# Optimization experiments

Hardware: AMD Instinct MI355X
Metric: run time of the kernel (lower is better)

Reference implementation:

```python
import jax, jax.numpy as jnp
import numpy as np

B, T, C, NH, L, V = 2, 1024, 768, 12, 4, 50304
HS = C // NH  # 64


def _norm(x):
    # torch: (x - x.mean(-1)) / x.std(-1) with unbiased std (ddof=1)
    mu = jnp.mean(x, axis=-1, keepdims=True)
    sd = jnp.std(x, axis=-1, ddof=1, keepdims=True)
    return (x - mu) / sd


def setup_inputs() -> dict:
    key = jax.random.key(0)
    ks = jax.random.split(key, 8)
    idx = jax.random.randint(ks[0], (B, T), 0, V)
    wte = jax.random.normal(ks[1], (V, C), jnp.float32) * 0.02
    wpe = jax.random.normal(ks[2], (1024, C), jnp.float32) * 0.02
    c_attn_w = jax.random.normal(ks[3], (L, 3 * C, C), jnp.float32) * 0.02
    c_proj_w = jax.random.normal(ks[4], (L, C, C), jnp.float32) * 0.02
    w_decay = jax.random.uniform(ks[5], (L, C), jnp.float32)          # decay in [0,1)
    eta = jax.random.uniform(ks[6], (L, C), jnp.float32) * 0.01       # small, like 1/block_size init
    lm_head_w = jax.random.normal(ks[7], (V, C), jnp.float32) * 0.02
    return dict(idx=idx, wte=wte, wpe=wpe, c_attn_w=c_attn_w, c_proj_w=c_proj_w,
                w_decay=w_decay, eta=eta, lm_head_w=lm_head_w)


def _rwkv7_block(x, Wqkv, Wproj, wd, et):
    Bx, Tx, Cx = x.shape
    qkv = (x @ Wqkv.T).reshape(Bx, Tx, 3, NH, HS)
    qkv = _norm(qkv)
    # [T, B, nh, hs] each
    q = jnp.transpose(qkv[:, :, 0], (1, 0, 2, 3))
    k = jnp.transpose(qkv[:, :, 1], (1, 0, 2, 3))
    v = jnp.transpose(qkv[:, :, 2], (1, 0, 2, 3))
    q = jax.lax.erf(q)
    k = jax.lax.erf(k)
    wv = wd.reshape(NH, HS)   # decay per (head, channel i)
    ev = et.reshape(NH, HS)
    a = -k
    b = k * ev
    k_ = k * ev
    v_ = v

    def step(state, inp):
        q_t, a_t, b_t, k_t, v_t = inp
        # state: [B, nh, hs(i), hs(k)]
        sab = jnp.einsum('bhik,bhk,bhj->bhij', state, a_t, b_t)
        state = state * wv[None, :, :, None] + sab + jnp.einsum('bhj,bhi->bhij', k_t, v_t)
        out = jnp.einsum('bhj,bhij->bhi', q_t, state)
        return state, out

    state0 = jnp.zeros((Bx, NH, HS, HS), x.dtype)
    _, vt = jax.lax.scan(step, state0, (q, a, b, k_, v_))  # vt: [T, B, nh, hs]
    y = jnp.transpose(vt, (1, 0, 2, 3)).reshape(Bx, Tx, Cx) @ Wproj.T
    return x + y


def reference(idx, wte, wpe, c_attn_w, c_proj_w, w_decay, eta, lm_head_w):
    t = idx.shape[1]
    x = wte[idx] + wpe[:t][None]
    for l in range(L):
        x = _rwkv7_block(x, c_attn_w[l], c_proj_w[l], w_decay[l], eta[l])
    x = _norm(x)
    # targets=None path: logits for last position only
    logits = x[:, -1:, :] @ lm_head_w.T  # [B, 1, V]
    return logits
```

## Files before the change

kernel.cpp:

```cpp
#include <hip/hip_runtime.h>
#include <hip/hip_bf16.h>
#include <cmath>

using bf16   = __bf16;
using bf16x8 = __attribute__((ext_vector_type(8))) __bf16;
using bf16x4 = __attribute__((ext_vector_type(4))) __bf16;
using f32x4  = __attribute__((ext_vector_type(4))) float;
using u32x4  = __attribute__((ext_vector_type(4))) unsigned int;

__global__ __launch_bounds__(256) void prologue_kernel(const int* __restrict__ idx,
                                                       const float* __restrict__ wte,
                                                       const float* __restrict__ wpe,
                                                       const float* __restrict__ c_attn_w,
                                                       const float* __restrict__ c_proj_w,
                                                       float* __restrict__ xf,
                                                       bf16* __restrict__ xb,
                                                       bf16* __restrict__ WqB,
                                                       bf16* __restrict__ WpB) {
  const int bid = blockIdx.x, tid = threadIdx.x;
  if (bid < 2048) {
    int t = bid & 1023;
    int tok = idx[bid];
    const float* wr = wte + (long)tok * 768;
    const float* pr = wpe + (long)t * 768;
    for (int c = tid; c < 768; c += 256) {
      float v = wr[c] + pr[c];
      xf[(long)bid * 768 + c] = v;
      xb[(long)bid * 768 + c] = (bf16)v;
    }
  }
  const int n4a = 4 * 2304 * 768 / 4;
  for (int i = bid * 256 + tid; i < n4a; i += 4096 * 256) {
    f32x4 v = ((const f32x4*)c_attn_w)[i];
    bf16x4 o;
    o[0] = (bf16)v[0]; o[1] = (bf16)v[1]; o[2] = (bf16)v[2]; o[3] = (bf16)v[3];
    ((bf16x4*)WqB)[i] = o;
  }
  const int n4p = 4 * 768 * 768 / 4;
  for (int i = bid * 256 + tid; i < n4p; i += 4096 * 256) {
    f32x4 v = ((const f32x4*)c_proj_w)[i];
    bf16x4 o;
    o[0] = (bf16)v[0]; o[1] = (bf16)v[1]; o[2] = (bf16)v[2]; o[3] = (bf16)v[3];
    ((bf16x4*)WpB)[i] = o;
  }
}

__global__ __launch_bounds__(256) void gemmqkv_kernel(const bf16* __restrict__ A,
                                                      const bf16* __restrict__ W,
                                                      const float* __restrict__ eta_l,
                                                      bf16* __restrict__ qG,
                                                      bf16* __restrict__ aG,
                                                      bf16* __restrict__ bG,
                                                      float* __restrict__ vG) {
  __shared__ char ldsA[128 * 128];
  __shared__ char ldsB[128 * 128];
  const int tid = threadIdx.x;
  const int l = tid & 63, wid = tid >> 6;
  const int lr = l & 15, g = l >> 4;
  const int m0 = blockIdx.y * 128, n0 = blockIdx.x * 128;
  const int wm = wid >> 1, wn = wid & 1;
  const int K = 768;

  f32x4 acc[4][4];
#pragma unroll
  for (int i = 0; i < 4; ++i)
#pragma unroll
    for (int j = 0; j < 4; ++j) acc[i][j] = {0.f, 0.f, 0.f, 0.f};

  for (int k0 = 0; k0 < K; k0 += 32) {
    __syncthreads();
#pragma unroll
    for (int it = 0; it < 2; ++it) {
      int slot = tid + it * 256;
      int row = slot >> 2, q = slot & 3;
      u32x4 da = *(const u32x4*)(A + (long)(m0 + row) * K + k0 + q * 8);
      *(u32x4*)(ldsA + row * 128 + ((q * 16) ^ ((row & 7) << 4))) = da;
      u32x4 db = *(const u32x4*)(W + (long)(n0 + row) * K + k0 + q * 8);
      *(u32x4*)(ldsB + row * 128 + ((q * 16) ^ ((row & 7) << 4))) = db;
    }
    __syncthreads();
    bf16x8 af[4], bfr[4];
#pragma unroll
    for (int it = 0; it < 4; ++it) {
      int row = wm * 64 + it * 16 + lr;
      af[it] = *(const bf16x8*)(ldsA + row * 128 + ((16 * g) ^ ((row & 7) << 4)));
    }
#pragma unroll
    for (int jt = 0; jt < 4; ++jt) {
      int row = wn * 64 + jt * 16 + lr;
      bfr[jt] = *(const bf16x8*)(ldsB + row * 128 + ((16 * g) ^ ((row & 7) << 4)));
    }
#pragma unroll
    for (int it = 0; it < 4; ++it)
#pragma unroll
      for (int jt = 0; jt < 4; ++jt)
        acc[it][jt] = __builtin_amdgcn_mfma_f32_16x16x32_bf16(af[it], bfr[jt], acc[it][jt], 0, 0, 0);
  }

  const int gi = blockIdx.x * 2 + wn;
  const int s = gi / 12, h = gi - s * 12;
  float evc[4];
#pragma unroll
  for (int jt = 0; jt < 4; ++jt) evc[jt] = eta_l[h * 64 + jt * 16 + lr];

#pragma unroll
  for (int it = 0; it < 4; ++it) {
#pragma unroll
    for (int r = 0; r < 4; ++r) {
      int row = m0 + wm * 64 + it * 16 + g * 4 + r;
      int b = row >> 10, t = row & 1023;
      float x0 = acc[it][0][r], x1 = acc[it][1][r];
      float x2 = acc[it][2][r], x3 = acc[it][3][r];
      float sum = (x0 + x1) + (x2 + x3);
#pragma unroll
      for (int o = 8; o; o >>= 1) sum += __shfl_xor(sum, o);
      float mu = sum * (1.f / 64.f);
      float d0 = x0 - mu, d1 = x1 - mu, d2 = x2 - mu, d3 = x3 - mu;
      float v2 = (d0 * d0 + d1 * d1) + (d2 * d2 + d3 * d3);
#pragma unroll
      for (int o = 8; o; o >>= 1) v2 += __shfl_xor(v2, o);
      float sd = sqrtf(v2 * (1.f / 63.f));
      float gn0 = d0 / sd, gn1 = d1 / sd, gn2 = d2 / sd, gn3 = d3 / sd;
      long base = ((long)(b * 12 + h) * 1024 + t) * 64 + lr;
      if (s == 0) {
        qG[base]      = (bf16)erff(gn0);
        qG[base + 16] = (bf16)erff(gn1);
        qG[base + 32] = (bf16)erff(gn2);
        qG[base + 48] = (bf16)erff(gn3);
      } else if (s == 1) {
        float k0 = erff(gn0), k1 = erff(gn1), k2 = erff(gn2), k3 = erff(gn3);
        aG[base]      = (bf16)(-k0);
        aG[base + 16] = (bf16)(-k1);
        aG[base + 32] = (bf16)(-k2);
        aG[base + 48] = (bf16)(-k3);
        bG[base]      = (bf16)(k0 * evc[0]);
        bG[base + 16] = (bf16)(k1 * evc[1]);
        bG[base + 32] = (bf16)(k2 * evc[2]);
        bG[base + 48] = (bf16)(k3 * evc[3]);
      } else {
        vG[base]      = gn0;
        vG[base + 16] = gn1;
        vG[base + 32] = gn2;
        vG[base + 48] = gn3;
      }
    }
  }
}

__global__ __launch_bounds__(256) void gemmproj_kernel(const bf16* __restrict__ A,
                                                       const bf16* __restrict__ W,
                                                       float* __restrict__ xf,
                                                       bf16* __restrict__ xb) {
  __shared__ char ldsA[128 * 128];
  __shared__ char ldsB[128 * 128];
  const int tid = threadIdx.x;
  const int l = tid & 63, wid = tid >> 6;
  const int lr = l & 15, g = l >> 4;
  const int m0 = blockIdx.y * 128, n0 = blockIdx.x * 128;
  const int wm = wid >> 1, wn = wid & 1;
  const int K = 768;

  f32x4 acc[4][4];
#pragma unroll
  for (int i = 0; i < 4; ++i)
#pragma unroll
    for (int j = 0; j < 4; ++j) acc[i][j] = {0.f, 0.f, 0.f, 0.f};

  for (int k0 = 0; k0 < K; k0 += 32) {
    __syncthreads();
#pragma unroll
    for (int it = 0; it < 2; ++it) {
      int slot = tid + it * 256;
      int row = slot >> 2, q = slot & 3;
      u32x4 da = *(const u32x4*)(A + (long)(m0 + row) * K + k0 + q * 8);
      *(u32x4*)(ldsA + row * 128 + ((q * 16) ^ ((row & 7) << 4))) = da;
      u32x4 db = *(const u32x4*)(W + (long)(n0 + row) * K + k0 + q * 8);
      *(u32x4*)(ldsB + row * 128 + ((q * 16) ^ ((row & 7) << 4))) = db;
    }
    __syncthreads();
    bf16x8 af[4], bfr[4];
#pragma unroll
    for (int it = 0; it < 4; ++it) {
      int row = wm * 64 + it * 16 + lr;
      af[it] = *(const bf16x8*)(ldsA + row * 128 + ((16 * g) ^ ((row & 7) << 4)));
    }
#pragma unroll
    for (int jt = 0; jt < 4; ++jt) {
      int row = wn * 64 + jt * 16 + lr;
      bfr[jt] = *(const bf16x8*)(ldsB + row * 128 + ((16 * g) ^ ((row & 7) << 4)));
    }
#pragma unroll
    for (int it = 0; it < 4; ++it)
#pragma unroll
      for (int jt = 0; jt < 4; ++jt)
        acc[it][jt] = __builtin_amdgcn_mfma_f32_16x16x32_bf16(af[it], bfr[jt], acc[it][jt], 0, 0, 0);
  }

#pragma unroll
  for (int it = 0; it < 4; ++it) {
#pragma unroll
    for (int jt = 0; jt < 4; ++jt) {
      int col = n0 + wn * 64 + jt * 16 + lr;
#pragma unroll
      for (int r = 0; r < 4; ++r) {
        int row = m0 + wm * 64 + it * 16 + g * 4 + r;
        long o = (long)row * 768 + col;
        float v = acc[it][jt][r] + xf[o];
        xf[o] = v;
        xb[o] = (bf16)v;
      }
    }
  }
}

__global__ __launch_bounds__(256) void gram_kernel(const bf16* __restrict__ aG,
                                                   const bf16* __restrict__ bG,
                                                   const bf16* __restrict__ qG,
                                                   float* __restrict__ GaG,
                                                   bf16* __restrict__ GqG,
                                                   bf16* __restrict__ bTG) {
  const int bh = blockIdx.x >> 6, ch = blockIdx.x & 63;
  __shared__ float as[16][68], bs[16][68], qs[16][68];
  const long tb = ((long)bh * 1024 + ch * 16) * 64;
  for (int i = threadIdx.x; i < 1024; i += 256) {
    int t = i >> 6, d = i & 63;
    as[t][d] = (float)aG[tb + i];
    bs[t][d] = (float)bG[tb + i];
    qs[t][d] = (float)qG[tb + i];
  }
  __syncthreads();
  const int t = threadIdx.x & 15, u = threadIdx.x >> 4;
  float dba = 0.f, dbq = 0.f;
#pragma unroll 4
  for (int d = 0; d < 64; ++d) {
    float bv = bs[u][d];
    dba += bv * as[t][d];
    dbq += bv * qs[t][d];
  }
  long g2 = (long)bh * 64 + ch;
  GaG[g2 * 256 + u * 16 + t] = (u < t) ? dba : 0.f;
  GqG[g2 * 512 + t * 32 + u] = (u <= t) ? (bf16)dbq : (bf16)0.f;
  GqG[g2 * 512 + t * 32 + 16 + u] = (bf16)0.f;
  int jj = threadIdx.x >> 2, uq = threadIdx.x & 3;
  bf16x8 pkv;
#pragma unroll
  for (int uu = 0; uu < 8; ++uu) pkv[uu] = (uq < 2) ? (bf16)bs[uq * 8 + uu][jj] : (bf16)0.f;
  *(bf16x8*)(bTG + g2 * 2048 + jj * 32 + uq * 8) = pkv;
}

__global__ __launch_bounds__(256) void scan_kernel(const float* __restrict__ wdl,
                                                   const bf16* __restrict__ aG,
                                                   const bf16* __restrict__ qG,
                                                   const float* __restrict__ vG,
                                                   const float* __restrict__ GaG,
                                                   const bf16* __restrict__ GqG,
                                                   const bf16* __restrict__ bTG,
                                                   bf16* __restrict__ yG) {
  const int bh = blockIdx.x;
  const int b = bh / 12, h = bh - b * 12;
  const int tid = threadIdx.x;
  const int l = tid & 63, wid = tid >> 6;
  const int lr = l & 15, g = l >> 4;

  __shared__ char sA[2][2][16 * 128];
  __shared__ char sQ[2][2][16 * 128];
  __shared__ char sB[2][2][64 * 64];
  __shared__ char sG[2][2][16 * 64];
  __shared__ float sGa[2][2][16][16];
  __shared__ float sV[2][2][16][64];
  __shared__ char sS[64 * 128];
  __shared__ float sM[16][68];

  const float* wrow = wdl + h * 64;
  const int irow = wid * 16 + lr;
  const float w_rec = fmaxf(wrow[irow], 0.004f);
  const float winv = 1.0f / w_rec;

  float wc[4], w15c[4], l2wc[4];
#pragma unroll
  for (int r = 0; r < 4; ++r) {
    int row = wid * 16 + g * 4 + r;
    float w = fmaxf(wrow[row], 0.004f);
    wc[r] = w;
    l2wc[r] = log2f(w);
    w15c[r] = exp2f(15.0f * l2wc[r]);
  }

  f32x4 Sf[4];
#pragma unroll
  for (int j = 0; j < 4; ++j) Sf[j] = {0.f, 0.f, 0.f, 0.f};

  const long hTD = (long)bh * 65536;
  const long gB = (long)bh * 64;

  u32x4 rAQ[2], rB[2], rGG[2];
  f32x4 rV[2];

  auto LOAD2 = [&](int c0) {
#pragma unroll
    for (int k = 0; k < 2; ++k) {
      const int c = c0 + k;
      const long tb = hTD + (long)c * 1024;
      if (tid < 128) {
        rAQ[k] = *(const u32x4*)(aG + tb + (tid >> 3) * 64 + (tid & 7) * 8);
      } else {
        rAQ[k] = *(const u32x4*)(qG + tb + ((tid - 128) >> 3) * 64 + ((tid - 128) & 7) * 8);
      }
      rB[k] = *(const u32x4*)(bTG + (gB + c) * 2048 + (tid >> 2) * 32 + (tid & 3) * 8);
      if (tid < 64) {
        rGG[k] = *(const u32x4*)(GqG + (gB + c) * 512 + (tid >> 2) * 32 + (tid & 3) * 8);
      } else if (tid < 128) {
        rGG[k] = *(const u32x4*)(GaG + (gB + c) * 256 + ((tid - 64) >> 2) * 16 + ((tid - 64) & 3) * 4);
      }
      rV[k] = *(const f32x4*)(vG + tb + (tid >> 4) * 64 + (tid & 15) * 4);
    }
  };

  auto STORE2 = [&](int nb) {
#pragma unroll
    for (int k = 0; k < 2; ++k) {
      if (tid < 128) {
        int t = tid >> 3, q = tid & 7;
        *(u32x4*)(sA[nb][k] + t * 128 + ((q * 16) ^ ((t & 7) << 4))) = rAQ[k];
      } else {
        int t = (tid - 128) >> 3, q = (tid - 128) & 7;
        *(u32x4*)(sQ[nb][k] + t * 128 + ((q * 16) ^ ((t & 7) << 4))) = rAQ[k];
      }
      {
        int j = tid >> 2, q = tid & 3;
        *(u32x4*)(sB[nb][k] + j * 64 + ((q * 16) ^ ((j & 3) << 4))) = rB[k];
      }
      if (tid < 64) {
        int t = tid >> 2, q = tid & 3;
        *(u32x4*)(sG[nb][k] + t * 64 + ((q * 16) ^ ((t & 3) << 4))) = rGG[k];
      } else if (tid < 128) {
        int u = (tid - 64) >> 2, q = (tid - 64) & 3;
        *(u32x4*)(&sGa[nb][k][u][q * 4]) = rGG[k];
      }
      {
        int t = tid >> 4, i4 = tid & 15;
        *(f32x4*)(&sV[nb][k][t][i4 * 4]) = rV[k];
      }
    }
  };

  auto COMPUTE = [&](int cur, int cip, int ch) {
    const char* pA = sA[cur][cip];
    const char* pQ = sQ[cur][cip];
    const char* pB = sB[cur][cip];
    const char* pG = sG[cur][cip];
    const float* pGa = &sGa[cur][cip][0][0];
    const float* pV = &sV[cur][cip][0][0] + irow;
    const float* pM = &sM[0][0] + irow;

    asm volatile("s_waitcnt lgkmcnt(0)" ::: "memory");
    __builtin_amdgcn_sched_barrier(0);

    f32x4 mf = {0.f, 0.f, 0.f, 0.f}, mqf = {0.f, 0.f, 0.f, 0.f};
#pragma unroll
    for (int s = 0; s < 2; ++s) {
      bf16x8 af = *(const bf16x8*)(sS + irow * 128 + ((64 * s + 16 * g) ^ ((irow & 7) << 4)));
      bf16x8 ba = *(const bf16x8*)(pA + lr * 128 + ((64 * s + 16 * g) ^ ((lr & 7) << 4)));
      bf16x8 bq = *(const bf16x8*)(pQ + lr * 128 + ((64 * s + 16 * g) ^ ((lr & 7) << 4)));
      mf = __builtin_amdgcn_mfma_f32_16x16x32_bf16(af, ba, mf, 0, 0, 0);
      mqf = __builtin_amdgcn_mfma_f32_16x16x32_bf16(af, bq, mqf, 0, 0, 0);
    }
#pragma unroll
    for (int r = 0; r < 4; ++r) sM[lr][wid * 16 + g * 4 + r] = mf[r];
    asm volatile("s_waitcnt lgkmcnt(0)" ::: "memory");
    __builtin_amdgcn_sched_barrier(0);

    f32x4 acc4[4];
#pragma unroll
    for (int t = 0; t < 4; ++t) acc4[t] = {0.f, 0.f, 0.f, 0.f};
    bf16x8 zfrag;
#pragma unroll
    for (int i = 0; i < 8; ++i) zfrag[i] = (bf16)0.0f;
    float wp = 1.f, wpm1 = 0.f, wiv = 1.f;
#pragma unroll
    for (int u = 0; u < 16; ++u) {
      float muv = pM[u * 68];
      float vu = pV[u * 64];
      float cc = wp * muv + wpm1 * acc4[u >> 2][u & 3];
      float zt = wiv * (cc + vu);
      zfrag[u & 7] = (g == (u >> 3)) ? (bf16)zt : zfrag[u & 7];
      f32x4 ztv = {zt, zt, zt, zt};
#pragma unroll
      for (int qq = 0; qq < 4; ++qq) {
        f32x4 ga = *(const f32x4*)(pGa + u * 16 + qq * 4);
        acc4[qq] = __builtin_elementwise_fma(ga, ztv, acc4[qq]);
      }
      wpm1 = wp;
      wp *= w_rec;
      wiv *= winv;
    }

#pragma unroll
    for (int jt = 0; jt < 4; ++jt) {
      int jrow = jt * 16 + lr;
      bf16x8 bb = *(const bf16x8*)(pB + jrow * 64 + ((16 * g) ^ ((jrow & 3) << 4)));
      f32x4 cs;
#pragma unroll
      for (int r = 0; r < 4; ++r) cs[r] = Sf[jt][r] * wc[r];
      f32x4 ns = __builtin_amdgcn_mfma_f32_16x16x32_bf16(zfrag, bb, cs, 0, 0, 0);
#pragma unroll
      for (int r = 0; r < 4; ++r) Sf[jt][r] = ns[r] * w15c[r];
    }

#pragma unroll
    for (int jt = 0; jt < 4; ++jt) {
#pragma unroll
      for (int r = 0; r < 4; ++r) {
        int row = wid * 16 + g * 4 + r;
        int d = jt * 16 + lr;
        *(bf16*)(sS + row * 128 + ((d * 2) ^ ((row & 7) << 4))) = (bf16)Sf[jt][r];
      }
    }

    {
      bf16x8 gq = *(const bf16x8*)(pG + lr * 64 + ((16 * g) ^ ((lr & 3) << 4)));
      f32x4 cy;
#pragma unroll
      for (int r = 0; r < 4; ++r) cy[r] = mqf[r] * wc[r];
      f32x4 yp = __builtin_amdgcn_mfma_f32_16x16x32_bf16(zfrag, gq, cy, 0, 0, 0);
      bf16x4 yo;
#pragma unroll
      for (int r = 0; r < 4; ++r) yo[r] = (bf16)(yp[r] * exp2f((float)lr * l2wc[r]));
      long yoff = ((long)b * 1024 + ch * 16 + lr) * 768 + h * 64 + wid * 16 + g * 4;
      *(bf16x4*)(yG + yoff) = yo;
    }
  };

  LOAD2(0);
  STORE2(0);
#pragma unroll
  for (int jt = 0; jt < 4; ++jt) {
#pragma unroll
    for (int r = 0; r < 4; ++r) {
      int row = wid * 16 + g * 4 + r;
      int d = jt * 16 + lr;
      *(bf16*)(sS + row * 128 + ((d * 2) ^ ((row & 7) << 4))) = (bf16)0.0f;
    }
  }
  __syncthreads();

  for (int gp = 0; gp < 32; ++gp) {
    const int cur = gp & 1;
    if (gp < 31) LOAD2(2 * gp + 2);
    COMPUTE(cur, 0, 2 * gp);
    COMPUTE(cur, 1, 2 * gp + 1);
    if (gp < 31) STORE2(cur ^ 1);
    __syncthreads();
  }
}

__global__ __launch_bounds__(256) void lmhead_kernel(const float* __restrict__ W,
                                                     const float* __restrict__ xf,
                                                     float* __restrict__ out) {
  __shared__ float xn[2][768];
  __shared__ float red[4];
  const int tid = threadIdx.x;
  for (int b = 0; b < 2; ++b) {
    const float* xr = xf + ((long)b * 1024 + 1023) * 768;
    float s = 0.f;
    for (int c = tid; c < 768; c += 256) s += xr[c];
#pragma unroll
    for (int o = 32; o; o >>= 1) s += __shfl_xor(s, o);
    if ((tid & 63) == 0) red[tid >> 6] = s;
    __syncthreads();
    float mu = (red[0] + red[1] + red[2] + red[3]) * (1.f / 768.f);
    __syncthreads();
    float s2 = 0.f;
    for (int c = tid; c < 768; c += 256) {
      float d = xr[c] - mu;
      s2 += d * d;
    }
#pragma unroll
    for (int o = 32; o; o >>= 1) s2 += __shfl_xor(s2, o);
    if ((tid & 63) == 0) red[tid >> 6] = s2;
    __syncthreads();
    float sd = sqrtf((red[0] + red[1] + red[2] + red[3]) * (1.f / 767.f));
    for (int c = tid; c < 768; c += 256) xn[b][c] = (xr[c] - mu) / sd;
    __syncthreads();
  }

  int l = tid & 63, wid = tid >> 6;
  int v0 = blockIdx.x * 64 + wid * 16;
  f32x4 x0[3], x1[3];
#pragma unroll
  for (int i = 0; i < 3; ++i) {
    x0[i] = *(const f32x4*)(&xn[0][l * 4 + i * 256]);
    x1[i] = *(const f32x4*)(&xn[1][l * 4 + i * 256]);
  }
  for (int vi = 0; vi < 16; ++vi) {
    const float* wr = W + (long)(v0 + vi) * 768;
    float pa = 0.f, pb = 0.f;
#pragma unroll
    for (int i = 0; i < 3; ++i) {
      f32x4 wv = *(const f32x4*)(wr + l * 4 + i * 256);
#pragma unroll
      for (int r = 0; r < 4; ++r) {
        pa += wv[r] * x0[i][r];
        pb += wv[r] * x1[i][r];
      }
    }
#pragma unroll
    for (int o = 32; o; o >>= 1) {
      pa += __shfl_xor(pa, o);
      pb += __shfl_xor(pb, o);
    }
    if (l == 0) {
      out[v0 + vi] = pa;
      out[50304 + v0 + vi] = pb;
    }
  }
}

extern "C" void kernel_launch(void* const* d_in, const int* in_sizes, int n_in,
                              void* d_out, int out_size, void* d_ws, size_t ws_size,
                              hipStream_t stream) {
  (void)in_sizes; (void)n_in; (void)out_size; (void)ws_size;
  const int*   idx      = (const int*)d_in[0];
  const float* wte      = (const float*)d_in[1];
  const float* wpe      = (const float*)d_in[2];
  const float* c_attn_w = (const float*)d_in[3];
  const float* c_proj_w = (const float*)d_in[4];
  const float* w_decay  = (const float*)d_in[5];
  const float* eta      = (const float*)d_in[6];
  const float* lm_head  = (const float*)d_in[7];
  float* out = (float*)d_out;

  char* ws = (char*)d_ws;
  size_t off = 0;
  auto alloc = [&](size_t bytes) -> char* {
    char* p = ws + off;
    off = (off + bytes + 255) & ~(size_t)255;
    return p;
  };
  float* xf   = (float*)alloc(2L * 1024 * 768 * 4);
  bf16*  xb   = (bf16*)alloc(2L * 1024 * 768 * 2);
  bf16*  qGp  = (bf16*)alloc(24L * 1024 * 64 * 2);
  bf16*  aGp  = (bf16*)alloc(24L * 1024 * 64 * 2);
  bf16*  bGp  = (bf16*)alloc(24L * 1024 * 64 * 2);
  float* vGp  = (float*)alloc(24L * 1024 * 64 * 4);
  float* GaGp = (float*)alloc(24L * 64 * 256 * 4);
  bf16*  GqGp = (bf16*)alloc(24L * 64 * 512 * 2);
  bf16*  bTGp = (bf16*)alloc(24L * 64 * 2048 * 2);
  bf16*  yGp  = (bf16*)alloc(2L * 1024 * 768 * 2);
  bf16*  WqB  = (bf16*)alloc(4L * 2304 * 768 * 2);
  bf16*  WpB  = (bf16*)alloc(4L * 768 * 768 * 2);

  prologue_kernel<<<dim3(4096), dim3(256), 0, stream>>>(
      idx, wte, wpe, c_attn_w, c_proj_w, xf, xb, WqB, WpB);

  for (int l = 0; l < 4; ++l) {
    gemmqkv_kernel<<<dim3(18, 16), dim3(256), 0, stream>>>(
        xb, WqB + (long)l * 2304 * 768, eta + l * 768, qGp, aGp, bGp, vGp);
    gram_kernel<<<dim3(1536), dim3(256), 0, stream>>>(aGp, bGp, qGp, GaGp, GqGp, bTGp);
    scan_kernel<<<dim3(24), dim3(256), 0, stream>>>(
        w_decay + l * 768, aGp, qGp, vGp, GaGp, GqGp, bTGp, yGp);
    gemmproj_kernel<<<dim3(6, 16), dim3(256), 0, stream>>>(
        yGp, WpB + (long)l * 768 * 768, xf, xb);
  }

  lmhead_kernel<<<dim3(786), dim3(256), 0, stream>>>(lm_head, xf, out);
}
```

Baseline: 781.3 us.

## Load scan operands directly into MFMA fragments and drop per-chunk block barriers

```diff
diff --git a/kernel.cpp b/kernel.cpp
--- a/kernel.cpp
+++ b/kernel.cpp
@@ -51,7 +51,7 @@
                                                       bf16* __restrict__ qG,
                                                       bf16* __restrict__ aG,
                                                       bf16* __restrict__ bG,
-                                                      float* __restrict__ vG) {
+                                                      float* __restrict__ vT) {
   __shared__ char ldsA[128 * 128];
   __shared__ char ldsB[128 * 128];
   const int tid = threadIdx.x;
@@ -138,10 +138,12 @@
         bG[base + 32] = (bf16)(k2 * evc[2]);
         bG[base + 48] = (bf16)(k3 * evc[3]);
       } else {
-        vG[base]      = gn0;
-        vG[base + 16] = gn1;
-        vG[base + 32] = gn2;
-        vG[base + 48] = gn3;
+        long cb = ((long)(b * 12 + h) * 64 + (t >> 4)) * 1024;
+        int u = t & 15;
+        vT[cb + (lr)      * 16 + u] = gn0;
+        vT[cb + (16 + lr) * 16 + u] = gn1;
+        vT[cb + (32 + lr) * 16 + u] = gn2;
+        vT[cb + (48 + lr) * 16 + u] = gn3;
       }
     }
   }
@@ -251,7 +253,7 @@
 __global__ __launch_bounds__(256) void scan_kernel(const float* __restrict__ wdl,
                                                    const bf16* __restrict__ aG,
                                                    const bf16* __restrict__ qG,
-                                                   const float* __restrict__ vG,
+                                                   const float* __restrict__ vT,
                                                    const float* __restrict__ GaG,
                                                    const bf16* __restrict__ GqG,
                                                    const bf16* __restrict__ bTG,
@@ -262,14 +264,9 @@
   const int l = tid & 63, wid = tid >> 6;
   const int lr = l & 15, g = l >> 4;
 
-  __shared__ char sA[2][2][16 * 128];
-  __shared__ char sQ[2][2][16 * 128];
-  __shared__ char sB[2][2][64 * 64];
-  __shared__ char sG[2][2][16 * 64];
-  __shared__ float sGa[2][2][16][16];
-  __shared__ float sV[2][2][16][64];
-  __shared__ char sS[64 * 128];
+  __shared__ char  sS[64 * 128];
   __shared__ float sM[16][68];
+  __shared__ float sGaW[4][16][16];
 
   const float* wrow = wdl + h * 64;
   const int irow = wid * 16 + lr;
@@ -293,77 +290,46 @@
   const long hTD = (long)bh * 65536;
   const long gB = (long)bh * 64;
 
-  u32x4 rAQ[2], rB[2], rGG[2];
-  f32x4 rV[2];
-
-  auto LOAD2 = [&](int c0) {
-#pragma unroll
-    for (int k = 0; k < 2; ++k) {
-      const int c = c0 + k;
-      const long tb = hTD + (long)c * 1024;
-      if (tid < 128) {
-        rAQ[k] = *(const u32x4*)(aG + tb + (tid >> 3) * 64 + (tid & 7) * 8);
-      } else {
-        rAQ[k] = *(const u32x4*)(qG + tb + ((tid - 128) >> 3) * 64 + ((tid - 128) & 7) * 8);
-      }
-      rB[k] = *(const u32x4*)(bTG + (gB + c) * 2048 + (tid >> 2) * 32 + (tid & 3) * 8);
-      if (tid < 64) {
-        rGG[k] = *(const u32x4*)(GqG + (gB + c) * 512 + (tid >> 2) * 32 + (tid & 3) * 8);
-      } else if (tid < 128) {
-        rGG[k] = *(const u32x4*)(GaG + (gB + c) * 256 + ((tid - 64) >> 2) * 16 + ((tid - 64) & 3) * 4);
-      }
-      rV[k] = *(const f32x4*)(vG + tb + (tid >> 4) * 64 + (tid & 15) * 4);
-    }
+  struct Frag {
+    bf16x8 a0, a1, q0, q1, bt0, bt1, bt2, bt3, gq;
+    f32x4 v0, v1, v2, v3, ga;
   };
 
-  auto STORE2 = [&](int nb) {
-#pragma unroll
-    for (int k = 0; k < 2; ++k) {
-      if (tid < 128) {
-        int t = tid >> 3, q = tid & 7;
-        *(u32x4*)(sA[nb][k] + t * 128 + ((q * 16) ^ ((t & 7) << 4))) = rAQ[k];
-      } else {
-        int t = (tid - 128) >> 3, q = (tid - 128) & 7;
-        *(u32x4*)(sQ[nb][k] + t * 128 + ((q * 16) ^ ((t & 7) << 4))) = rAQ[k];
-      }
-      {
-        int j = tid >> 2, q = tid & 3;
-        *(u32x4*)(sB[nb][k] + j * 64 + ((q * 16) ^ ((j & 3) << 4))) = rB[k];
-      }
-      if (tid < 64) {
-        int t = tid >> 2, q = tid & 3;
-        *(u32x4*)(sG[nb][k] + t * 64 + ((q * 16) ^ ((t & 3) << 4))) = rGG[k];
-      } else if (tid < 128) {
-        int u = (tid - 64) >> 2, q = (tid - 64) & 3;
-        *(u32x4*)(&sGa[nb][k][u][q * 4]) = rGG[k];
-      }
-      {
-        int t = tid >> 4, i4 = tid & 15;
-        *(f32x4*)(&sV[nb][k][t][i4 * 4]) = rV[k];
-      }
-    }
+  auto LOADF = [&](int c, Frag& F) {
+    const long tb = hTD + (long)c * 1024;
+    const bf16* ap = aG + tb + lr * 64 + 8 * g;
+    F.a0 = *(const bf16x8*)(ap);
+    F.a1 = *(const bf16x8*)(ap + 32);
+    const bf16* qp = qG + tb + lr * 64 + 8 * g;
+    F.q0 = *(const bf16x8*)(qp);
+    F.q1 = *(const bf16x8*)(qp + 32);
+    const bf16* bp = bTG + (gB + c) * 2048 + lr * 32 + 8 * g;
+    F.bt0 = *(const bf16x8*)(bp);
+    F.bt1 = *(const bf16x8*)(bp + 512);
+    F.bt2 = *(const bf16x8*)(bp + 1024);
+    F.bt3 = *(const bf16x8*)(bp + 1536);
+    F.gq = *(const bf16x8*)(GqG + (gB + c) * 512 + lr * 32 + 8 * g);
+    const float* vp = vT + ((gB + c) * 64 + irow) * 16;
+    F.v0 = *(const f32x4*)(vp);
+    F.v1 = *(const f32x4*)(vp + 4);
+    F.v2 = *(const f32x4*)(vp + 8);
+    F.v3 = *(const f32x4*)(vp + 12);
+    F.ga = *(const f32x4*)(GaG + (gB + c) * 256 + l * 4);
   };
 
-  auto COMPUTE = [&](int cur, int cip, int ch) {
-    const char* pA = sA[cur][cip];
-    const char* pQ = sQ[cur][cip];
-    const char* pB = sB[cur][cip];
-    const char* pG = sG[cur][cip];
-    const float* pGa = &sGa[cur][cip][0][0];
-    const float* pV = &sV[cur][cip][0][0] + irow;
-    const float* pM = &sM[0][0] + irow;
-
+  auto COMPUTE = [&](int c, const Frag& F) {
+    *(f32x4*)(&sGaW[wid][l >> 2][(l & 3) * 4]) = F.ga;
     asm volatile("s_waitcnt lgkmcnt(0)" ::: "memory");
     __builtin_amdgcn_sched_barrier(0);
 
     f32x4 mf = {0.f, 0.f, 0.f, 0.f}, mqf = {0.f, 0.f, 0.f, 0.f};
-#pragma unroll
-    for (int s = 0; s < 2; ++s) {
-      bf16x8 af = *(const bf16x8*)(sS + irow * 128 + ((64 * s + 16 * g) ^ ((irow & 7) << 4)));
-      bf16x8 ba = *(const bf16x8*)(pA + lr * 128 + ((64 * s + 16 * g) ^ ((lr & 7) << 4)));
-      bf16x8 bq = *(const bf16x8*)(pQ + lr * 128 + ((64 * s + 16 * g) ^ ((lr & 7) << 4)));
-      mf = __builtin_amdgcn_mfma_f32_16x16x32_bf16(af, ba, mf, 0, 0, 0);
-      mqf = __builtin_amdgcn_mfma_f32_16x16x32_bf16(af, bq, mqf, 0, 0, 0);
+    {
+      bf16x8 af0 = *(const bf16x8*)(sS + irow * 128 + ((16 * g) ^ ((irow & 7) << 4)));
+      bf16x8 af1 = *(const bf16x8*)(sS + irow * 128 + ((64 + 16 * g) ^ ((irow & 7) << 4)));
+      mf = __builtin_amdgcn_mfma_f32_16x16x32_bf16(af0, F.a0, mf, 0, 0, 0);
+      mf = __builtin_amdgcn_mfma_f32_16x16x32_bf16(af1, F.a1, mf, 0, 0, 0);
+      mqf = __builtin_amdgcn_mfma_f32_16x16x32_bf16(af0, F.q0, mqf, 0, 0, 0);
+      mqf = __builtin_amdgcn_mfma_f32_16x16x32_bf16(af1, F.q1, mqf, 0, 0, 0);
     }
 #pragma unroll
     for (int r = 0; r < 4; ++r) sM[lr][wid * 16 + g * 4 + r] = mf[r];
@@ -379,15 +345,18 @@
     float wp = 1.f, wpm1 = 0.f, wiv = 1.f;
 #pragma unroll
     for (int u = 0; u < 16; ++u) {
-      float muv = pM[u * 68];
-      float vu = pV[u * 64];
+      float muv = sM[u][irow];
+      float vu = (u >> 2) == 0 ? F.v0[u & 3]
+               : (u >> 2) == 1 ? F.v1[u & 3]
+               : (u >> 2) == 2 ? F.v2[u & 3]
+               : F.v3[u & 3];
       float cc = wp * muv + wpm1 * acc4[u >> 2][u & 3];
       float zt = wiv * (cc + vu);
       zfrag[u & 7] = (g == (u >> 3)) ? (bf16)zt : zfrag[u & 7];
       f32x4 ztv = {zt, zt, zt, zt};
 #pragma unroll
       for (int qq = 0; qq < 4; ++qq) {
-        f32x4 ga = *(const f32x4*)(pGa + u * 16 + qq * 4);
+        f32x4 ga = *(const f32x4*)(&sGaW[wid][u][qq * 4]);
         acc4[qq] = __builtin_elementwise_fma(ga, ztv, acc4[qq]);
       }
       wpm1 = wp;
@@ -397,8 +366,7 @@
 
 #pragma unroll
     for (int jt = 0; jt < 4; ++jt) {
-      int jrow = jt * 16 + lr;
-      bf16x8 bb = *(const bf16x8*)(pB + jrow * 64 + ((16 * g) ^ ((jrow & 3) << 4)));
+      bf16x8 bb = jt == 0 ? F.bt0 : jt == 1 ? F.bt1 : jt == 2 ? F.bt2 : F.bt3;
       f32x4 cs;
 #pragma unroll
       for (int r = 0; r < 4; ++r) cs[r] = Sf[jt][r] * wc[r];
@@ -418,21 +386,20 @@
     }
 
     {
-      bf16x8 gq = *(const bf16x8*)(pG + lr * 64 + ((16 * g) ^ ((lr & 3) << 4)));
       f32x4 cy;
 #pragma unroll
       for (int r = 0; r < 4; ++r) cy[r] = mqf[r] * wc[r];
-      f32x4 yp = __builtin_amdgcn_mfma_f32_16x16x32_bf16(zfrag, gq, cy, 0, 0, 0);
+      f32x4 yp = __builtin_amdgcn_mfma_f32_16x16x32_bf16(zfrag, F.gq, cy, 0, 0, 0);
       bf16x4 yo;
 #pragma unroll
       for (int r = 0; r < 4; ++r) yo[r] = (bf16)(yp[r] * exp2f((float)lr * l2wc[r]));
-      long yoff = ((long)b * 1024 + ch * 16 + lr) * 768 + h * 64 + wid * 16 + g * 4;
+      long yoff = ((long)b * 1024 + c * 16 + lr) * 768 + h * 64 + wid * 16 + g * 4;
       *(bf16x4*)(yG + yoff) = yo;
     }
   };
 
-  LOAD2(0);
-  STORE2(0);
+  Frag FA, FB;
+  LOADF(0, FA);
 #pragma unroll
   for (int jt = 0; jt < 4; ++jt) {
 #pragma unroll
@@ -442,15 +409,12 @@
       *(bf16*)(sS + row * 128 + ((d * 2) ^ ((row & 7) << 4))) = (bf16)0.0f;
     }
   }
-  __syncthreads();
 
   for (int gp = 0; gp < 32; ++gp) {
-    const int cur = gp & 1;
-    if (gp < 31) LOAD2(2 * gp + 2);
-    COMPUTE(cur, 0, 2 * gp);
-    COMPUTE(cur, 1, 2 * gp + 1);
-    if (gp < 31) STORE2(cur ^ 1);
-    __syncthreads();
+    LOADF(2 * gp + 1, FB);
+    COMPUTE(2 * gp, FA);
+    if (gp < 31) LOADF(2 * gp + 2, FA);
+    COMPUTE(2 * gp + 1, FB);
   }
 }
 
@@ -542,7 +506,7 @@
   bf16*  qGp  = (bf16*)alloc(24L * 1024 * 64 * 2);
   bf16*  aGp  = (bf16*)alloc(24L * 1024 * 64 * 2);
   bf16*  bGp  = (bf16*)alloc(24L * 1024 * 64 * 2);
-  float* vGp  = (float*)alloc(24L * 1024 * 64 * 4);
+  float* vTp  = (float*)alloc(24L * 64 * 64 * 16 * 4);
   float* GaGp = (float*)alloc(24L * 64 * 256 * 4);
   bf16*  GqGp = (bf16*)alloc(24L * 64 * 512 * 2);
   bf16*  bTGp = (bf16*)alloc(24L * 64 * 2048 * 2);
@@ -555,10 +519,10 @@
 
   for (int l = 0; l < 4; ++l) {
     gemmqkv_kernel<<<dim3(18, 16), dim3(256), 0, stream>>>(
-        xb, WqB + (long)l * 2304 * 768, eta + l * 768, qGp, aGp, bGp, vGp);
+        xb, WqB + (long)l * 2304 * 768, eta + l * 768, qGp, aGp, bGp, vTp);
     gram_kernel<<<dim3(1536), dim3(256), 0, stream>>>(aGp, bGp, qGp, GaGp, GqGp, bTGp);
     scan_kernel<<<dim3(24), dim3(256), 0, stream>>>(
-        w_decay + l * 768, aGp, qGp, vGp, GaGp, GqGp, bTGp, yGp);
+        w_decay + l * 768, aGp, qGp, vTp, GaGp, GqGp, bTGp, yGp);
     gemmproj_kernel<<<dim3(6, 16), dim3(256), 0, stream>>>(
         yGp, WpB + (long)l * 768 * 768, xf, xb);
   }
```

Result: slower. 823.5 us (+5.4%).

## Double-buffer LDS tiles in QKV and projection GEMMs with register prefetch

Applied to the files above, without the earlier changes.

```diff
diff --git a/kernel.cpp b/kernel.cpp
--- a/kernel.cpp
+++ b/kernel.cpp
@@ -52,8 +52,8 @@
                                                       bf16* __restrict__ aG,
                                                       bf16* __restrict__ bG,
                                                       float* __restrict__ vG) {
-  __shared__ char ldsA[128 * 128];
-  __shared__ char ldsB[128 * 128];
+  __shared__ char ldsA[2][128 * 128];
+  __shared__ char ldsB[2][128 * 128];
   const int tid = threadIdx.x;
   const int l = tid & 63, wid = tid >> 6;
   const int lr = l & 15, g = l >> 4;
@@ -67,34 +67,52 @@
 #pragma unroll
     for (int j = 0; j < 4; ++j) acc[i][j] = {0.f, 0.f, 0.f, 0.f};
 
-  for (int k0 = 0; k0 < K; k0 += 32) {
-    __syncthreads();
+  u32x4 rA[2], rBv[2];
+  auto LOADG = [&](int k0) {
 #pragma unroll
     for (int it = 0; it < 2; ++it) {
       int slot = tid + it * 256;
       int row = slot >> 2, q = slot & 3;
-      u32x4 da = *(const u32x4*)(A + (long)(m0 + row) * K + k0 + q * 8);
-      *(u32x4*)(ldsA + row * 128 + ((q * 16) ^ ((row & 7) << 4))) = da;
-      u32x4 db = *(const u32x4*)(W + (long)(n0 + row) * K + k0 + q * 8);
-      *(u32x4*)(ldsB + row * 128 + ((q * 16) ^ ((row & 7) << 4))) = db;
-    }
-    __syncthreads();
+      rA[it] = *(const u32x4*)(A + (long)(m0 + row) * K + k0 + q * 8);
+      rBv[it] = *(const u32x4*)(W + (long)(n0 + row) * K + k0 + q * 8);
+    }
+  };
+  auto STOREL = [&](int nb) {
+#pragma unroll
+    for (int it = 0; it < 2; ++it) {
+      int slot = tid + it * 256;
+      int row = slot >> 2, q = slot & 3;
+      *(u32x4*)(ldsA[nb] + row * 128 + ((q * 16) ^ ((row & 7) << 4))) = rA[it];
+      *(u32x4*)(ldsB[nb] + row * 128 + ((q * 16) ^ ((row & 7) << 4))) = rBv[it];
+    }
+  };
+
+  LOADG(0);
+  STOREL(0);
+  __syncthreads();
+
+  const int nk = K / 32;
+  for (int kk = 0; kk < nk; ++kk) {
+    const int cur = kk & 1;
+    if (kk + 1 < nk) LOADG((kk + 1) * 32);
     bf16x8 af[4], bfr[4];
 #pragma unroll
     for (int it = 0; it < 4; ++it) {
       int row = wm * 64 + it * 16 + lr;
-      af[it] = *(const bf16x8*)(ldsA + row * 128 + ((16 * g) ^ ((row & 7) << 4)));
+      af[it] = *(const bf16x8*)(ldsA[cur] + row * 128 + ((16 * g) ^ ((row & 7) << 4)));
     }
 #pragma unroll
     for (int jt = 0; jt < 4; ++jt) {
       int row = wn * 64 + jt * 16 + lr;
-      bfr[jt] = *(const bf16x8*)(ldsB + row * 128 + ((16 * g) ^ ((row & 7) << 4)));
+      bfr[jt] = *(const bf16x8*)(ldsB[cur] + row * 128 + ((16 * g) ^ ((row & 7) << 4)));
     }
 #pragma unroll
     for (int it = 0; it < 4; ++it)
 #pragma unroll
       for (int jt = 0; jt < 4; ++jt)
         acc[it][jt] = __builtin_amdgcn_mfma_f32_16x16x32_bf16(af[it], bfr[jt], acc[it][jt], 0, 0, 0);
+    if (kk + 1 < nk) STOREL(cur ^ 1);
+    __syncthreads();
   }
 
   const int gi = blockIdx.x * 2 + wn;
@@ -151,8 +169,8 @@
                                                        const bf16* __restrict__ W,
                                                        float* __restrict__ xf,
                                                        bf16* __restrict__ xb) {
-  __shared__ char ldsA[128 * 128];
-  __shared__ char ldsB[128 * 128];
+  __shared__ char ldsA[2][128 * 128];
+  __shared__ char ldsB[2][128 * 128];
   const int tid = threadIdx.x;
   const int l = tid & 63, wid = tid >> 6;
   const int lr = l & 15, g = l >> 4;
@@ -166,34 +184,52 @@
 #pragma unroll
     for (int j = 0; j < 4; ++j) acc[i][j] = {0.f, 0.f, 0.f, 0.f};
 
-  for (int k0 = 0; k0 < K; k0 += 32) {
-    __syncthreads();
+  u32x4 rA[2], rBv[2];
+  auto LOADG = [&](int k0) {
 #pragma unroll
     for (int it = 0; it < 2; ++it) {
       int slot = tid + it * 256;
       int row = slot >> 2, q = slot & 3;
-      u32x4 da = *(const u32x4*)(A + (long)(m0 + row) * K + k0 + q * 8);
-      *(u32x4*)(ldsA + row * 128 + ((q * 16) ^ ((row & 7) << 4))) = da;
-      u32x4 db = *(const u32x4*)(W + (long)(n0 + row) * K + k0 + q * 8);
-      *(u32x4*)(ldsB + row * 128 + ((q * 16) ^ ((row & 7) << 4))) = db;
-    }
-    __syncthreads();
+      rA[it] = *(const u32x4*)(A + (long)(m0 + row) * K + k0 + q * 8);
+      rBv[it] = *(const u32x4*)(W + (long)(n0 + row) * K + k0 + q * 8);
+    }
+  };
+  auto STOREL = [&](int nb) {
+#pragma unroll
+    for (int it = 0; it < 2; ++it) {
+      int slot = tid + it * 256;
+      int row = slot >> 2, q = slot & 3;
+      *(u32x4*)(ldsA[nb] + row * 128 + ((q * 16) ^ ((row & 7) << 4))) = rA[it];
+      *(u32x4*)(ldsB[nb] + row * 128 + ((q * 16) ^ ((row & 7) << 4))) = rBv[it];
+    }
+  };
+
+  LOADG(0);
+  STOREL(0);
+  __syncthreads();
+
+  const int nk = K / 32;
+  for (int kk = 0; kk < nk; ++kk) {
+    const int cur = kk & 1;
+    if (kk + 1 < nk) LOADG((kk + 1) * 32);
     bf16x8 af[4], bfr[4];
 #pragma unroll
     for (int it = 0; it < 4; ++it) {
       int row = wm * 64 + it * 16 + lr;
-      af[it] = *(const bf16x8*)(ldsA + row * 128 + ((16 * g) ^ ((row & 7) << 4)));
+      af[it] = *(const bf16x8*)(ldsA[cur] + row * 128 + ((16 * g) ^ ((row & 7) << 4)));
     }
 #pragma unroll
     for (int jt = 0; jt < 4; ++jt) {
       int row = wn * 64 + jt * 16 + lr;
-      bfr[jt] = *(const bf16x8*)(ldsB + row * 128 + ((16 * g) ^ ((row & 7) << 4)));
+      bfr[jt] = *(const bf16x8*)(ldsB[cur] + row * 128 + ((16 * g) ^ ((row & 7) << 4)));
     }
 #pragma unroll
     for (int it = 0; it < 4; ++it)
 #pragma unroll
       for (int jt = 0; jt < 4; ++jt)
         acc[it][jt] = __builtin_amdgcn_mfma_f32_16x16x32_bf16(af[it], bfr[jt], acc[it][jt], 0, 0, 0);
+    if (kk + 1 < nk) STOREL(cur ^ 1);
+    __syncthreads();
   }
 
 #pragma unroll
```

Result: faster. 765.9 us (-2.0%).
